# Performance work log

Hardware: AMD Instinct MI355X
Metric: run time of the kernel (lower is better)

Reference implementation:

```python
import jax, jax.numpy as jnp
import numpy as np

HEADS = 8
DEPTH = 2
LN_EPS = 1e-5


def _layernorm(x, g, b):
    m = jnp.mean(x, axis=-1, keepdims=True)
    v = jnp.var(x, axis=-1, keepdims=True)
    return (x - m) / jnp.sqrt(v + LN_EPS) * g + b


def setup_inputs() -> dict:
    key = jax.random.key(0)
    ks = jax.random.split(key, 16)
    b, c, n, t = 4, 64, 512, 12
    L, H = DEPTH, 256  # depth, mlp_dim
    s = 0.05
    return {
        'x': jax.random.normal(ks[0], (b, c, n, t), jnp.float32),
        'adj': jax.random.uniform(ks[1], (n, n), jnp.float32) / n,
        'pos': 0.02 * jax.random.normal(ks[2], (1, n, c), jnp.float32),
        'qkv_w': s * jax.random.normal(ks[3], (L, 3 * c, c), jnp.float32),
        'proj_w': s * jax.random.normal(ks[4], (L, c, c), jnp.float32),
        'proj_b': jnp.zeros((L, c), jnp.float32),
        'ln_g': jnp.ones((L, c), jnp.float32),
        'ln_b': jnp.zeros((L, c), jnp.float32),
        'ff_w1': s * jax.random.normal(ks[5], (L, H, c), jnp.float32),
        'ff_b1': jnp.zeros((L, H), jnp.float32),
        'ff_w2': s * jax.random.normal(ks[6], (L, c, H), jnp.float32),
        'ff_b2': jnp.zeros((L, c), jnp.float32),
        'gcn_w': s * jax.random.normal(ks[7], (L, c, 3 * c), jnp.float32),  # Conv2d 1x1: [c_out, 3*c_in]
        'gcn_b': jnp.zeros((L, c), jnp.float32),
    }


def reference(x, adj, pos, qkv_w, proj_w, proj_b, ln_g, ln_b,
              ff_w1, ff_b1, ff_w2, ff_b2, gcn_w, gcn_b):
    b, c, n, t = x.shape
    hd = c // HEADS
    scale = hd ** (-0.5)
    # [b, c, n, t] -> [b*t, n, c]
    h = jnp.transpose(x, (0, 3, 2, 1)).reshape(b * t, n, c) + pos
    for l in range(DEPTH):
        residual = h.reshape(b, t, n, c)
        # --- manual MHA (no pre-norm around attention, faithful to source) ---
        qkv = jnp.einsum('bnc,oc->bno', h, qkv_w[l])  # [bt, n, 3c]
        qkv = qkv.reshape(b * t, n, 3, HEADS, hd).transpose(2, 0, 3, 1, 4)
        q, k, v = qkv[0], qkv[1], qkv[2]  # [bt, heads, n, hd]
        attn = jax.nn.softmax(jnp.einsum('bhnd,bhmd->bhnm', q, k) * scale, axis=-1)
        o = jnp.einsum('bhnm,bhmd->bhnd', attn, v)
        o = o.transpose(0, 2, 1, 3).reshape(b * t, n, c)
        o = jnp.einsum('bnc,oc->bno', o, proj_w[l]) + proj_b[l]
        h = o + h
        # --- PreNorm FeedForward ---
        y = _layernorm(h, ln_g[l], ln_b[l])
        y = jax.nn.gelu(jnp.einsum('bnc,hc->bnh', y, ff_w1[l]) + ff_b1[l], approximate=False)
        y = jnp.einsum('bnh,ch->bnc', y, ff_w2[l]) + ff_b2[l]
        h = y + h
        # --- GCN on residual (order=2 diffusion) ---
        r = jnp.transpose(residual, (0, 3, 2, 1))  # [b, c, n, t]
        x1 = jnp.einsum('bcvt,vw->bcwt', r, adj)
        x2 = jnp.einsum('bcvt,vw->bcwt', x1, adj)
        cat = jnp.concatenate([r, x1, x2], axis=1)  # [b, 3c, n, t]
        g = jnp.einsum('bknt,ok->bont', cat, gcn_w[l]) + gcn_b[l][None, :, None, None]
        h = jnp.transpose(g, (0, 3, 2, 1)).reshape(b * t, n, c) + h
    return jnp.transpose(h.reshape(b, t, n, c), (0, 3, 2, 1))
```

## Files before the change

### kernel.cpp

```cpp
#include <hip/hip_runtime.h>
#include <math.h>


typedef __fp16 half_t;
typedef __attribute__((ext_vector_type(2))) __fp16 half2v;
typedef __attribute__((ext_vector_type(4))) __fp16 half4v;
typedef __attribute__((ext_vector_type(4))) float f32x4;

union PU  { half2v h2[2]; half4v h4; };
union F4H { float4 f; half4v h[2]; };
union F2H { float2 f2; half4v h4; };

#define ATS 72
#define BTS 68
#define KLS 20
#define QLS 20
#define VTS 516

__global__ __launch_bounds__(256) void k_pre(const float* __restrict__ x,
                                             const float* __restrict__ pos,
                                             const float* __restrict__ adj,
                                             const float* __restrict__ qkv_w,
                                             const float* __restrict__ proj_w,
                                             const float* __restrict__ ff_w1,
                                             const float* __restrict__ ff_w2,
                                             const float* __restrict__ gcn_w,
                                             float* __restrict__ h,
                                             half_t* __restrict__ hh,
                                             half_t* __restrict__ adjTh,
                                             half_t* __restrict__ wh,
                                             half_t* __restrict__ adjT2h) {
    __shared__ __align__(16) char smem[17920];
    float* t = (float*)smem;
    int tid = threadIdx.x;
    int bidx = blockIdx.x;
    if (bidx < 384) {
        int b = bidx / 96, vt0 = (bidx % 96) * 64;
#pragma unroll
        for (int i = 0; i < 4; ++i) {
            int g = tid + i * 256;
            int r = g >> 4, q = g & 15;
            *(float4*)&t[r * 65 + 4 * q] =
                *(const float4*)(x + ((size_t)(b * 64 + r)) * 6144 + vt0 + 4 * q);
        }
        __syncthreads();
#pragma unroll
        for (int i = 0; i < 4; ++i) {
            int g = tid + i * 256;
            int r = g >> 4, q = g & 15;
            int vt = vt0 + r;
            int v = vt / 12, tt = vt - v * 12;
            float4 pv = *(const float4*)(pos + v * 64 + 4 * q);
            float4 o;
            o.x = t[(4 * q + 0) * 65 + r] + pv.x;
            o.y = t[(4 * q + 1) * 65 + r] + pv.y;
            o.z = t[(4 * q + 2) * 65 + r] + pv.z;
            o.w = t[(4 * q + 3) * 65 + r] + pv.w;
            size_t idx = ((size_t)((b * 12 + tt) * 512 + v)) * 64 + 4 * q;
            *(float4*)(h + idx) = o;
            PU u;
            u.h2[0] = __builtin_amdgcn_cvt_pkrtz(o.x, o.y);
            u.h2[1] = __builtin_amdgcn_cvt_pkrtz(o.z, o.w);
            *(half4v*)(hh + idx) = u.h4;
        }
    } else if (bidx < 448) {
        int fb = bidx - 384;
        int v0 = (fb & 7) * 64, w0 = (fb >> 3) * 64;
#pragma unroll
        for (int i = 0; i < 4; ++i) {
            int g = tid + i * 256;
            int r = g >> 4, q = g & 15;
            float4 a = *(const float4*)(adj + (size_t)(v0 + r) * 512 + w0 + 4 * q);
            t[(4 * q + 0) * 65 + r] = a.x;
            t[(4 * q + 1) * 65 + r] = a.y;
            t[(4 * q + 2) * 65 + r] = a.z;
            t[(4 * q + 3) * 65 + r] = a.w;
        }
        __syncthreads();
#pragma unroll
        for (int i = 0; i < 4; ++i) {
            int g = tid + i * 256;
            int rw = g >> 4, q = g & 15;
            const float* src = &t[rw * 65 + 4 * q];
            PU u;
            u.h2[0] = __builtin_amdgcn_cvt_pkrtz(src[0], src[1]);
            u.h2[1] = __builtin_amdgcn_cvt_pkrtz(src[2], src[3]);
            *(half4v*)(adjTh + (size_t)(w0 + rw) * 512 + v0 + 4 * q) = u.h4;
        }
    } else if (bidx < 928) {
        int i = (bidx - 448) * 256 + tid;
        float v;
        if (i < 24576) v = qkv_w[i];
        else if (i < 32768) v = proj_w[i - 24576];
        else if (i < 65536) v = ff_w1[i - 32768];
        else if (i < 98304) v = ff_w2[i - 65536];
        else v = gcn_w[i - 98304];
        wh[i] = (half_t)v;
    } else {
        half_t* a_t = (half_t*)smem;
        half_t* b_t = (half_t*)smem + 64 * ATS;
        int fb = bidx - 928;
        int w0 = (fb & 7) * 64, v0 = (fb >> 3) * 64;
        int wave = tid >> 6, lane = tid & 63;
        int lm = lane & 15, lg = lane >> 4;
        const f32x4 zc = {0.f, 0.f, 0.f, 0.f};
        f32x4 acc[4] = {zc, zc, zc, zc};
        for (int kc = 0; kc < 8; ++kc) {
#pragma unroll
            for (int i = 0; i < 4; ++i) {
                int g = tid + i * 256;
                int uu = g >> 4, q = g & 15;
                float4 a = *(const float4*)(adj + (size_t)(kc * 64 + uu) * 512 + w0 + 4 * q);
                a_t[(4 * q + 0) * ATS + uu] = (half_t)a.x;
                a_t[(4 * q + 1) * ATS + uu] = (half_t)a.y;
                a_t[(4 * q + 2) * ATS + uu] = (half_t)a.z;
                a_t[(4 * q + 3) * ATS + uu] = (half_t)a.w;
            }
#pragma unroll
            for (int i = 0; i < 4; ++i) {
                int g = tid + i * 256;
                int c = g >> 4, q = g & 15;
                float4 a = *(const float4*)(adj + (size_t)(v0 + c) * 512 + kc * 64 + 4 * q);
                PU u;
                u.h2[0] = __builtin_amdgcn_cvt_pkrtz(a.x, a.y);
                u.h2[1] = __builtin_amdgcn_cvt_pkrtz(a.z, a.w);
                *(half4v*)&b_t[c * BTS + 4 * q] = u.h4;
            }
            __syncthreads();
#pragma unroll
            for (int k16 = 0; k16 < 4; ++k16) {
                half4v af = *(const half4v*)&a_t[(wave * 16 + lm) * ATS + k16 * 16 + lg * 4];
#pragma unroll
                for (int nt = 0; nt < 4; ++nt) {
                    half4v bf = *(const half4v*)&b_t[(nt * 16 + lm) * BTS + k16 * 16 + lg * 4];
                    acc[nt] = __builtin_amdgcn_mfma_f32_16x16x16f16(af, bf, acc[nt], 0, 0, 0);
                }
            }
            __syncthreads();
        }
#pragma unroll
        for (int nt = 0; nt < 4; ++nt)
#pragma unroll
            for (int r = 0; r < 4; ++r)
                adjT2h[(size_t)(w0 + wave * 16 + lg * 4 + r) * 512 + v0 + nt * 16 + lm] =
                    (half_t)acc[nt][r];
    }
}

__global__ __launch_bounds__(256) void k_qd(const half_t* __restrict__ hh,
                                            const half_t* __restrict__ Wh,
                                            half_t* __restrict__ qh,
                                            half_t* __restrict__ kh,
                                            half_t* __restrict__ vh,
                                            const half_t* __restrict__ adjTh,
                                            const half_t* __restrict__ adjT2h,
                                            half_t* __restrict__ x1h,
                                            half_t* __restrict__ x2h) {
    __shared__ __align__(16) half_t sbuf[2 * 64 * ATS + 64 * BTS];
    int tid = threadIdx.x;
    int bidx = blockIdx.x;
    int wave = tid >> 6, lane = tid & 63;
    int lm = lane & 15, lg = lane >> 4;
    const f32x4 zc = {0.f, 0.f, 0.f, 0.f};

    if (bidx < 384) {
        int wid = bidx * 4 + wave;
        int row = wid * 16 + lm;
        half4v xf[4];
#pragma unroll
        for (int kc = 0; kc < 4; ++kc) {
            F2H u;
            u.f2 = *(const float2*)(hh + (size_t)row * 64 + kc * 16 + lg * 4);
            xf[kc] = u.h4;
        }
        const float SC = 0.35355339059327373f * 1.4426950408889634f;
        int bt = row >> 9, v = row & 511;
        half4v wf[4];
#pragma unroll
        for (int kc = 0; kc < 4; ++kc)
            wf[kc] = *(const half4v*)(Wh + (size_t)lm * 64 + kc * 16 + lg * 4);
#pragma unroll
        for (int nt = 0; nt < 12; ++nt) {
            half4v cw[4];
#pragma unroll
            for (int kc = 0; kc < 4; ++kc) cw[kc] = wf[kc];
            if (nt < 11) {
#pragma unroll
                for (int kc = 0; kc < 4; ++kc)
                    wf[kc] = *(const half4v*)(Wh + (size_t)((nt + 1) * 16 + lm) * 64 + kc * 16 + lg * 4);
            }
            f32x4 acc = zc;
#pragma unroll
            for (int kc = 0; kc < 4; ++kc)
                acc = __builtin_amdgcn_mfma_f32_16x16x16f16(cw[kc], xf[kc], acc, 0, 0, 0);
            int s = nt >> 2;
            if (s == 0) { acc[0] *= SC; acc[1] *= SC; acc[2] *= SC; acc[3] *= SC; }
            int head = ((nt & 3) << 1) + (lg >> 1);
            int d0 = (lg & 1) * 4;
            PU o2;
            o2.h2[0] = __builtin_amdgcn_cvt_pkrtz(acc[0], acc[1]);
            o2.h2[1] = __builtin_amdgcn_cvt_pkrtz(acc[2], acc[3]);
            half_t* dst = (s == 0) ? qh : ((s == 1) ? kh : vh);
            *(half4v*)(dst + ((size_t)(bt * 8 + head) * 512 + v) * 8 + d0) = o2.h4;
        }
    } else {
        half_t* a_t  = sbuf;
        half_t* a2_t = sbuf + 64 * ATS;
        half_t* b_t  = sbuf + 2 * 64 * ATS;
        int fb = bidx - 384;
        int w0 = (fb & 7) * 64;
        int bt = fb >> 3;
        f32x4 acc0[4] = {zc, zc, zc, zc};
        f32x4 acc1[4] = {zc, zc, zc, zc};
        for (int kc = 0; kc < 8; ++kc) {
#pragma unroll
            for (int i = 0; i < 4; ++i) {
                int g = tid + i * 256;
                if (g < 512) {
                    int r = g >> 3, s = g & 7;
                    *(float4*)&a_t[r * ATS + s * 8] =
                        *(const float4*)(adjTh + (size_t)(w0 + r) * 512 + kc * 64 + s * 8);
                } else {
                    int g2 = g - 512;
                    int r = g2 >> 3, s = g2 & 7;
                    *(float4*)&a2_t[r * ATS + s * 8] =
                        *(const float4*)(adjT2h + (size_t)(w0 + r) * 512 + kc * 64 + s * 8);
                }
            }
#pragma unroll
            for (int i = 0; i < 2; ++i) {
                int g = tid + i * 256;
                int vr = g >> 3, s = g & 7;
                F4H u;
                u.f = *(const float4*)(hh + ((size_t)(bt * 512 + kc * 64 + vr)) * 64 + s * 8);
#pragma unroll
                for (int e = 0; e < 8; ++e)
                    b_t[(s * 8 + e) * BTS + vr] = u.h[e >> 2][e & 3];
            }
            __syncthreads();
#pragma unroll
            for (int k16 = 0; k16 < 4; ++k16) {
                half4v af0 = *(const half4v*)&a_t[(wave * 16 + lm) * ATS + k16 * 16 + lg * 4];
                half4v af1 = *(const half4v*)&a2_t[(wave * 16 + lm) * ATS + k16 * 16 + lg * 4];
#pragma unroll
                for (int nt = 0; nt < 4; ++nt) {
                    half4v bf = *(const half4v*)&b_t[(nt * 16 + lm) * BTS + k16 * 16 + lg * 4];
                    acc0[nt] = __builtin_amdgcn_mfma_f32_16x16x16f16(af0, bf, acc0[nt], 0, 0, 0);
                    acc1[nt] = __builtin_amdgcn_mfma_f32_16x16x16f16(af1, bf, acc1[nt], 0, 0, 0);
                }
            }
            __syncthreads();
        }
#pragma unroll
        for (int nt = 0; nt < 4; ++nt)
#pragma unroll
            for (int r = 0; r < 4; ++r) {
                size_t o = (size_t)(w0 + wave * 16 + lg * 4 + r) * 3072 + bt * 64 + nt * 16 + lm;
                x1h[o] = (half_t)acc0[nt][r];
                x2h[o] = (half_t)acc1[nt][r];
            }
    }
}

__global__ __launch_bounds__(512) void k_ag(const half_t* __restrict__ qh,
                                            const half_t* __restrict__ kh,
                                            const half_t* __restrict__ vh,
                                            half_t* __restrict__ obh,
                                            const half_t* __restrict__ hh,
                                            const half_t* __restrict__ x1h,
                                            const half_t* __restrict__ x2h,
                                            const half_t* __restrict__ Wh,
                                            const float* __restrict__ bias,
                                            float* __restrict__ gout) {
    __shared__ __align__(16) half_t sbuf[512 * KLS + 16 * VTS + 256 * QLS];
    int tid = threadIdx.x;
    int bidx = blockIdx.x;
    const half4v zero4 = {(__fp16)0.f, (__fp16)0.f, (__fp16)0.f, (__fp16)0.f};
    const f32x4 zc = {0.f, 0.f, 0.f, 0.f};

    if (bidx < 768) {
        half_t* kl = sbuf;
        half_t* vt = sbuf + 512 * KLS;
        half_t* ql = sbuf + 512 * KLS + 16 * VTS;
        int bh = bidx >> 1;
        int half_ = bidx & 1;
        const half_t* kbase = kh + (size_t)bh * 4096;
        const half_t* vbase = vh + (size_t)bh * 4096;
        const half_t* qbase = qh + (size_t)bh * 4096 + half_ * 2048;

        if (tid < 256) {
#pragma unroll
            for (int kk = 0; kk < 2; ++kk) {
                int key = tid * 2 + kk;
                F4H u;
                u.f = *(const float4*)(kbase + key * 8);
                half4v* rowp = (half4v*)&kl[key * KLS];
                rowp[0] = u.h[0];
                rowp[1] = u.h[1];
                rowp[2] = zero4;
                rowp[3] = zero4;
            }
            {
                F4H u;
                u.f = *(const float4*)(qbase + tid * 8);
                half4v* rowp = (half4v*)&ql[tid * QLS];
                rowp[0] = u.h[0];
                rowp[1] = u.h[1];
                rowp[2] = zero4;
                rowp[3] = zero4;
            }
            {
                int k0 = tid * 2;
                F4H a, b;
                a.f = *(const float4*)(vbase + k0 * 8);
                b.f = *(const float4*)(vbase + k0 * 8 + 8);
#pragma unroll
                for (int d = 0; d < 8; ++d) {
                    half2v p = {a.h[d >> 2][d & 3], b.h[d >> 2][d & 3]};
                    *(half2v*)&vt[d * VTS + k0] = p;
                }
            }
        }
        for (int i = tid; i < 1032; i += 512)
            ((half4v*)(vt + 8 * VTS))[i] = zero4;
        __syncthreads();

        int wave = tid >> 6, lane = tid & 63;
        int lm = lane & 15, lg = lane >> 4;
        int bt = bh >> 3, head = bh & 7;

#pragma unroll 1
        for (int st = 0; st < 2; ++st) {
            int qrow0 = wave * 32 + st * 16;
            half4v qf = *(const half4v*)&ql[(qrow0 + lm) * QLS + lg * 4];
            f32x4 acc = zc;
            float l0 = 0.f, l1 = 0.f, l2 = 0.f, l3 = 0.f;
#pragma unroll 4
            for (int kt = 0; kt < 32; ++kt) {
                int key0 = kt * 16;
                half4v ka = *(const half4v*)&kl[(key0 + lm) * KLS + lg * 4];
                f32x4 c1 = __builtin_amdgcn_mfma_f32_16x16x16f16(ka, qf, zc, 0, 0, 0);
                float p0 = exp2f(fminf(c1[0], 12.f));
                float p1 = exp2f(fminf(c1[1], 12.f));
                float p2 = exp2f(fminf(c1[2], 12.f));
                float p3 = exp2f(fminf(c1[3], 12.f));
                l0 += p0; l1 += p1; l2 += p2; l3 += p3;
                PU pu;
                pu.h2[0] = __builtin_amdgcn_cvt_pkrtz(p0, p1);
                pu.h2[1] = __builtin_amdgcn_cvt_pkrtz(p2, p3);
                half4v va = *(const half4v*)&vt[lm * VTS + key0 + lg * 4];
                acc = __builtin_amdgcn_mfma_f32_16x16x16f16(va, pu.h4, acc, 0, 0, 0);
            }
            float lsum = (l0 + l1) + (l2 + l3);
            lsum += __shfl_xor(lsum, 16);
            lsum += __shfl_xor(lsum, 32);
            if (lg < 2) {
                float inv = 1.f / lsum;
                int rowg = half_ * 256 + qrow0 + lm;
                PU o2;
                o2.h2[0] = __builtin_amdgcn_cvt_pkrtz(acc[0] * inv, acc[1] * inv);
                o2.h2[1] = __builtin_amdgcn_cvt_pkrtz(acc[2] * inv, acc[3] * inv);
                *(half4v*)(obh + ((size_t)(bt * 512 + rowg)) * 64 + head * 8 + lg * 4) = o2.h4;
            }
        }
    } else {
        half_t* a_t = sbuf;
        half_t* b_t = sbuf + 64 * ATS;
        int row0 = (bidx - 768) * 64;
        int wave = tid >> 6, lane = tid & 63;
        int lm = lane & 15, lg = lane >> 4;
        f32x4 acc[4] = {zc, zc, zc, zc};

        for (int ch = 0; ch < 3; ++ch) {
            if (tid < 256) {
                if (ch == 0) {
#pragma unroll
                    for (int i = 0; i < 2; ++i) {
                        int g = tid + i * 256;
                        int r = g >> 3, s = g & 7;
                        int rowg = row0 + r;
                        int v = rowg / 48, bt = rowg - v * 48;
                        *(float4*)&a_t[r * ATS + s * 8] =
                            *(const float4*)(hh + ((size_t)(bt * 512 + v)) * 64 + s * 8);
                    }
                } else {
                    const half_t* X = (ch == 1) ? x1h : x2h;
#pragma unroll
                    for (int i = 0; i < 2; ++i) {
                        int g = tid + i * 256;
                        int r = g >> 3, s = g & 7;
                        *(float4*)&a_t[r * ATS + s * 8] =
                            *(const float4*)(X + (size_t)(row0 + r) * 64 + s * 8);
                    }
                }
#pragma unroll
                for (int i = 0; i < 4; ++i) {
                    int g = tid + i * 256;
                    int r = g >> 4, q = g & 15;
                    *(half4v*)&b_t[r * BTS + 4 * q] =
                        *(const half4v*)(Wh + (size_t)r * 192 + ch * 64 + 4 * q);
                }
            }
            __syncthreads();
            if (tid < 256) {
#pragma unroll
                for (int k16 = 0; k16 < 4; ++k16) {
                    half4v af = *(const half4v*)&a_t[(wave * 16 + lm) * ATS + k16 * 16 + lg * 4];
#pragma unroll
                    for (int nt = 0; nt < 4; ++nt) {
                        half4v bf = *(const half4v*)&b_t[(nt * 16 + lm) * BTS + k16 * 16 + lg * 4];
                        acc[nt] = __builtin_amdgcn_mfma_f32_16x16x16f16(bf, af, acc[nt], 0, 0, 0);
                    }
                }
            }
            __syncthreads();
        }
        if (tid < 256) {
            int row = row0 + wave * 16 + lm;
            int v = row / 48, bt = row - v * 48;
            float* gp = gout + ((size_t)(bt * 512 + v)) * 64;
#pragma unroll
            for (int nt = 0; nt < 4; ++nt) {
                float4 bb = *(const float4*)(bias + nt * 16 + lg * 4);
                *(float4*)(gp + nt * 16 + lg * 4) =
                    make_float4(acc[nt][0] + bb.x, acc[nt][1] + bb.y,
                                acc[nt][2] + bb.z, acc[nt][3] + bb.w);
            }
        }
    }
}

__global__ __launch_bounds__(128) void k_plf(const half_t* __restrict__ obh,
                                             const half_t* __restrict__ pwh,
                                             const float* __restrict__ pb,
                                             const float* __restrict__ g,
                                             const float* __restrict__ bln,
                                             const half_t* __restrict__ w1h,
                                             const float* __restrict__ b1,
                                             const half_t* __restrict__ w2h,
                                             const float* __restrict__ b2,
                                             const float* __restrict__ gout,
                                             float* __restrict__ h,
                                             half_t* __restrict__ hh,
                                             float* __restrict__ out,
                                             int last) {
    int wid = blockIdx.x * 2 + (threadIdx.x >> 6);
    int lane = threadIdx.x & 63;
    int lm = lane & 15, lg = lane >> 4;
    int row = wid * 16 + lm;
    const f32x4 zc = {0.f, 0.f, 0.f, 0.f};

    half4v pf[4];
#pragma unroll
    for (int kc = 0; kc < 4; ++kc)
        pf[kc] = *(const half4v*)(pwh + (size_t)lm * 64 + kc * 16 + lg * 4);

    half4v of[4];
#pragma unroll
    for (int kc = 0; kc < 4; ++kc) {
        F2H u;
        u.f2 = *(const float2*)(obh + (size_t)row * 64 + kc * 16 + lg * 4);
        of[kc] = u.h4;
    }

    f32x4 hp[4];
#pragma unroll
    for (int nt = 0; nt < 4; ++nt) {
        half4v cw[4];
#pragma unroll
        for (int kc = 0; kc < 4; ++kc) cw[kc] = pf[kc];
        if (nt < 3) {
#pragma unroll
            for (int kc = 0; kc < 4; ++kc)
                pf[kc] = *(const half4v*)(pwh + (size_t)((nt + 1) * 16 + lm) * 64 + kc * 16 + lg * 4);
        }
        f32x4 c = zc;
#pragma unroll
        for (int kc = 0; kc < 4; ++kc)
            c = __builtin_amdgcn_mfma_f32_16x16x16f16(cw[kc], of[kc], c, 0, 0, 0);
        float4 ho = *(const float4*)(h + (size_t)row * 64 + nt * 16 + lg * 4);
        float4 bb = *(const float4*)(pb + nt * 16 + lg * 4);
        hp[nt][0] = c[0] + ho.x + bb.x;
        hp[nt][1] = c[1] + ho.y + bb.y;
        hp[nt][2] = c[2] + ho.z + bb.z;
        hp[nt][3] = c[3] + ho.w + bb.w;
    }

    float s = 0.f, s2 = 0.f;
#pragma unroll
    for (int nt = 0; nt < 4; ++nt)
#pragma unroll
        for (int r = 0; r < 4; ++r) {
            s += hp[nt][r];
            s2 += hp[nt][r] * hp[nt][r];
        }
    s += __shfl_xor(s, 16);  s2 += __shfl_xor(s2, 16);
    s += __shfl_xor(s, 32);  s2 += __shfl_xor(s2, 32);
    float mean = s * (1.f / 64.f);
    float var = s2 * (1.f / 64.f) - mean * mean;
    float rstd = rsqrtf(var + 1e-5f);

    half4v xf[4];
#pragma unroll
    for (int nt = 0; nt < 4; ++nt) {
        float4 gg = *(const float4*)(g + nt * 16 + lg * 4);
        float4 bb = *(const float4*)(bln + nt * 16 + lg * 4);
        float y0 = (hp[nt][0] - mean) * rstd * gg.x + bb.x;
        float y1 = (hp[nt][1] - mean) * rstd * gg.y + bb.y;
        float y2 = (hp[nt][2] - mean) * rstd * gg.z + bb.z;
        float y3 = (hp[nt][3] - mean) * rstd * gg.w + bb.w;
        PU u;
        u.h2[0] = __builtin_amdgcn_cvt_pkrtz(y0, y1);
        u.h2[1] = __builtin_amdgcn_cvt_pkrtz(y2, y3);
        xf[nt] = u.h4;
    }

    half4v w1f[4];
#pragma unroll
    for (int kc = 0; kc < 4; ++kc)
        w1f[kc] = *(const half4v*)(w1h + (size_t)lm * 64 + kc * 16 + lg * 4);

    f32x4 acc[4] = {zc, zc, zc, zc};
#pragma unroll 4
    for (int ht = 0; ht < 16; ++ht) {
        half4v cw[4];
#pragma unroll
        for (int kc = 0; kc < 4; ++kc) cw[kc] = w1f[kc];
        half4v w2f[4];
#pragma unroll
        for (int ot = 0; ot < 4; ++ot)
            w2f[ot] = *(const half4v*)(w2h + (size_t)(ot * 16 + lm) * 256 + ht * 16 + lg * 4);
        if (ht < 15) {
#pragma unroll
            for (int kc = 0; kc < 4; ++kc)
                w1f[kc] = *(const half4v*)(w1h + (size_t)((ht + 1) * 16 + lm) * 64 + kc * 16 + lg * 4);
        }
        f32x4 c1 = zc;
#pragma unroll
        for (int kc = 0; kc < 4; ++kc)
            c1 = __builtin_amdgcn_mfma_f32_16x16x16f16(cw[kc], xf[kc], c1, 0, 0, 0);
        float4 bb = *(const float4*)(b1 + ht * 16 + lg * 4);
        float y0 = c1[0] + bb.x;
        float y1 = c1[1] + bb.y;
        float y2 = c1[2] + bb.z;
        float y3 = c1[3] + bb.w;
        y0 = 0.5f * y0 * (1.0f + erff(y0 * 0.70710678118654752f));
        y1 = 0.5f * y1 * (1.0f + erff(y1 * 0.70710678118654752f));
        y2 = 0.5f * y2 * (1.0f + erff(y2 * 0.70710678118654752f));
        y3 = 0.5f * y3 * (1.0f + erff(y3 * 0.70710678118654752f));
        PU p;
        p.h2[0] = __builtin_amdgcn_cvt_pkrtz(y0, y1);
        p.h2[1] = __builtin_amdgcn_cvt_pkrtz(y2, y3);
#pragma unroll
        for (int ot = 0; ot < 4; ++ot)
            acc[ot] = __builtin_amdgcn_mfma_f32_16x16x16f16(w2f[ot], p.h4, acc[ot], 0, 0, 0);
    }

    if (!last) {
#pragma unroll
        for (int ot = 0; ot < 4; ++ot) {
            float4 bb = *(const float4*)(b2 + ot * 16 + lg * 4);
            float4 gv = *(const float4*)(gout + (size_t)row * 64 + ot * 16 + lg * 4);
            float4 fv = make_float4(hp[ot][0] + acc[ot][0] + bb.x + gv.x,
                                    hp[ot][1] + acc[ot][1] + bb.y + gv.y,
                                    hp[ot][2] + acc[ot][2] + bb.z + gv.z,
                                    hp[ot][3] + acc[ot][3] + bb.w + gv.w);
            size_t idx = (size_t)row * 64 + ot * 16 + lg * 4;
            *(float4*)(h + idx) = fv;
            PU u;
            u.h2[0] = __builtin_amdgcn_cvt_pkrtz(fv.x, fv.y);
            u.h2[1] = __builtin_amdgcn_cvt_pkrtz(fv.z, fv.w);
            *(half4v*)(hh + idx) = u.h4;
        }
    } else {
        int bt = row >> 9, v = row & 511;
        int b = bt / 12, t = bt - b * 12;
        float* op = out + (size_t)b * 393216 + v * 12 + t;
#pragma unroll
        for (int ot = 0; ot < 4; ++ot) {
            float4 bb = *(const float4*)(b2 + ot * 16 + lg * 4);
            float4 gv = *(const float4*)(gout + (size_t)row * 64 + ot * 16 + lg * 4);
            int c0 = ot * 16 + lg * 4;
            op[(size_t)(c0 + 0) * 6144] = hp[ot][0] + acc[ot][0] + bb.x + gv.x;
            op[(size_t)(c0 + 1) * 6144] = hp[ot][1] + acc[ot][1] + bb.y + gv.y;
            op[(size_t)(c0 + 2) * 6144] = hp[ot][2] + acc[ot][2] + bb.z + gv.z;
            op[(size_t)(c0 + 3) * 6144] = hp[ot][3] + acc[ot][3] + bb.w + gv.w;
        }
    }
}

extern "C" void kernel_launch(void* const* d_in, const int* in_sizes, int n_in,
                              void* d_out, int out_size, void* d_ws, size_t ws_size,
                              hipStream_t stream) {
    const float* x      = (const float*)d_in[0];
    const float* adj    = (const float*)d_in[1];
    const float* pos    = (const float*)d_in[2];
    const float* qkv_w  = (const float*)d_in[3];
    const float* proj_w = (const float*)d_in[4];
    const float* proj_b = (const float*)d_in[5];
    const float* ln_g   = (const float*)d_in[6];
    const float* ln_b   = (const float*)d_in[7];
    const float* ff_w1  = (const float*)d_in[8];
    const float* ff_b1  = (const float*)d_in[9];
    const float* ff_w2  = (const float*)d_in[10];
    const float* ff_b2  = (const float*)d_in[11];
    const float* gcn_w  = (const float*)d_in[12];
    const float* gcn_b  = (const float*)d_in[13];
    float* out = (float*)d_out;

    const size_t SZ = 1572864;
    float* h    = (float*)d_ws;
    float* gout = h + SZ;
    half_t* hh  = (half_t*)(gout + SZ);
    half_t* x1h = hh + SZ;
    half_t* x2h = x1h + SZ;
    half_t* qh  = x2h + SZ;
    half_t* kh  = qh + SZ;
    half_t* vh  = kh + SZ;
    half_t* obh = vh + SZ;
    half_t* adjTh  = obh + SZ;
    half_t* adjT2h = adjTh + 262144;
    half_t* wh     = adjT2h + 262144;
    half_t* qkv_wh  = wh;
    half_t* proj_wh = wh + 24576;
    half_t* ff_w1h  = wh + 32768;
    half_t* ff_w2h  = wh + 65536;
    half_t* gcn_wh  = wh + 98304;

    k_pre<<<992, 256, 0, stream>>>(x, pos, adj, qkv_w, proj_w, ff_w1, ff_w2, gcn_w,
                                   h, hh, adjTh, wh, adjT2h);
    for (int l = 0; l < 2; ++l) {
        k_qd<<<768, 256, 0, stream>>>(hh, qkv_wh + l * 12288, qh, kh, vh,
                                      adjTh, adjT2h, x1h, x2h);
        k_ag<<<1152, 512, 0, stream>>>(qh, kh, vh, obh, hh, x1h, x2h,
                                       gcn_wh + l * 12288, gcn_b + l * 64, gout);
        k_plf<<<768, 128, 0, stream>>>(obh, proj_wh + l * 4096, proj_b + l * 64,
                                       ln_g + l * 64, ln_b + l * 64,
                                       ff_w1h + l * 16384, ff_b1 + l * 256,
                                       ff_w2h + l * 16384, ff_b2 + l * 64, gout, h, hh,
                                       out, l);
    }
}
```

Baseline: 275.3 us.

## Fuse GCN 1x1 conv into diffusion kernel and vectorize weight conversion

Fuses the GCN channel-mixing matmul into the adjacency diffusion blocks of k_qd. The x1/x2 tiles stay in shared memory next to the residual tile and are multiplied by the GCN weights directly, removing the x1h/x2h global round-trip and the separate GEMM blocks in k_ag. k_ag now only does attention with 768 blocks. The weight-to-fp16 conversion in k_pre is vectorized to float4, which cuts its block count. The trade-off is more shared memory and register pressure in k_qd, plus GCN weights read straight from global memory per block.

```diff
diff --git a/kernel.cpp b/kernel.cpp
--- a/kernel.cpp
+++ b/kernel.cpp
@@ -16,6 +16,7 @@
 #define KLS 20
 #define QLS 20
 #define VTS 516
+#define CTS 200
 
 __global__ __launch_bounds__(256) void k_pre(const float* __restrict__ x,
                                              const float* __restrict__ pos,
@@ -87,19 +88,22 @@
             u.h2[1] = __builtin_amdgcn_cvt_pkrtz(src[2], src[3]);
             *(half4v*)(adjTh + (size_t)(w0 + rw) * 512 + v0 + 4 * q) = u.h4;
         }
-    } else if (bidx < 928) {
-        int i = (bidx - 448) * 256 + tid;
-        float v;
-        if (i < 24576) v = qkv_w[i];
-        else if (i < 32768) v = proj_w[i - 24576];
-        else if (i < 65536) v = ff_w1[i - 32768];
-        else if (i < 98304) v = ff_w2[i - 65536];
-        else v = gcn_w[i - 98304];
-        wh[i] = (half_t)v;
+    } else if (bidx < 568) {
+        int i = ((bidx - 448) * 256 + tid) * 4;
+        float4 v;
+        if (i < 24576) v = *(const float4*)(qkv_w + i);
+        else if (i < 32768) v = *(const float4*)(proj_w + (i - 24576));
+        else if (i < 65536) v = *(const float4*)(ff_w1 + (i - 32768));
+        else if (i < 98304) v = *(const float4*)(ff_w2 + (i - 65536));
+        else v = *(const float4*)(gcn_w + (i - 98304));
+        PU u;
+        u.h2[0] = __builtin_amdgcn_cvt_pkrtz(v.x, v.y);
+        u.h2[1] = __builtin_amdgcn_cvt_pkrtz(v.z, v.w);
+        *(half4v*)(wh + i) = u.h4;
     } else {
         half_t* a_t = (half_t*)smem;
         half_t* b_t = (half_t*)smem + 64 * ATS;
-        int fb = bidx - 928;
+        int fb = bidx - 568;
         int w0 = (fb & 7) * 64, v0 = (fb >> 3) * 64;
         int wave = tid >> 6, lane = tid & 63;
         int lm = lane & 15, lg = lane >> 4;
@@ -154,8 +158,9 @@
                                             half_t* __restrict__ vh,
                                             const half_t* __restrict__ adjTh,
                                             const half_t* __restrict__ adjT2h,
-                                            half_t* __restrict__ x1h,
-                                            half_t* __restrict__ x2h) {
+                                            const half_t* __restrict__ Wg,
+                                            const float* __restrict__ gb,
+                                            float* __restrict__ gout) {
     __shared__ __align__(16) half_t sbuf[2 * 64 * ATS + 64 * BTS];
     int tid = threadIdx.x;
     int bidx = blockIdx.x;
@@ -251,181 +256,137 @@
             }
             __syncthreads();
         }
+        half_t* cat_t = sbuf;
 #pragma unroll
         for (int nt = 0; nt < 4; ++nt)
 #pragma unroll
             for (int r = 0; r < 4; ++r) {
-                size_t o = (size_t)(w0 + wave * 16 + lg * 4 + r) * 3072 + bt * 64 + nt * 16 + lm;
-                x1h[o] = (half_t)acc0[nt][r];
-                x2h[o] = (half_t)acc1[nt][r];
-            }
+                int vrow = wave * 16 + lg * 4 + r;
+                cat_t[vrow * CTS + 64  + nt * 16 + lm] = (half_t)acc0[nt][r];
+                cat_t[vrow * CTS + 128 + nt * 16 + lm] = (half_t)acc1[nt][r];
+            }
+#pragma unroll
+        for (int i = 0; i < 2; ++i) {
+            int g = tid + i * 256;
+            int r = g >> 3, s = g & 7;
+            *(float4*)&cat_t[r * CTS + s * 8] =
+                *(const float4*)(hh + ((size_t)(bt * 512 + w0 + r)) * 64 + s * 8);
+        }
+        __syncthreads();
+        f32x4 gacc[4] = {zc, zc, zc, zc};
+#pragma unroll
+        for (int k16 = 0; k16 < 12; ++k16) {
+            half4v cf = *(const half4v*)&cat_t[(wave * 16 + lm) * CTS + k16 * 16 + lg * 4];
+#pragma unroll
+            for (int nt = 0; nt < 4; ++nt) {
+                half4v wf = *(const half4v*)(Wg + (size_t)(nt * 16 + lm) * 192 + k16 * 16 + lg * 4);
+                gacc[nt] = __builtin_amdgcn_mfma_f32_16x16x16f16(wf, cf, gacc[nt], 0, 0, 0);
+            }
+        }
+        int grow = bt * 512 + w0 + wave * 16 + lm;
+        float* gp = gout + (size_t)grow * 64;
+#pragma unroll
+        for (int nt = 0; nt < 4; ++nt) {
+            float4 bb = *(const float4*)(gb + nt * 16 + lg * 4);
+            *(float4*)(gp + nt * 16 + lg * 4) =
+                make_float4(gacc[nt][0] + bb.x, gacc[nt][1] + bb.y,
+                            gacc[nt][2] + bb.z, gacc[nt][3] + bb.w);
+        }
     }
 }
 
 __global__ __launch_bounds__(512) void k_ag(const half_t* __restrict__ qh,
                                             const half_t* __restrict__ kh,
                                             const half_t* __restrict__ vh,
-                                            half_t* __restrict__ obh,
-                                            const half_t* __restrict__ hh,
-                                            const half_t* __restrict__ x1h,
-                                            const half_t* __restrict__ x2h,
-                                            const half_t* __restrict__ Wh,
-                                            const float* __restrict__ bias,
-                                            float* __restrict__ gout) {
+                                            half_t* __restrict__ obh) {
     __shared__ __align__(16) half_t sbuf[512 * KLS + 16 * VTS + 256 * QLS];
     int tid = threadIdx.x;
     int bidx = blockIdx.x;
     const half4v zero4 = {(__fp16)0.f, (__fp16)0.f, (__fp16)0.f, (__fp16)0.f};
     const f32x4 zc = {0.f, 0.f, 0.f, 0.f};
 
-    if (bidx < 768) {
-        half_t* kl = sbuf;
-        half_t* vt = sbuf + 512 * KLS;
-        half_t* ql = sbuf + 512 * KLS + 16 * VTS;
-        int bh = bidx >> 1;
-        int half_ = bidx & 1;
-        const half_t* kbase = kh + (size_t)bh * 4096;
-        const half_t* vbase = vh + (size_t)bh * 4096;
-        const half_t* qbase = qh + (size_t)bh * 4096 + half_ * 2048;
-
-        if (tid < 256) {
-#pragma unroll
-            for (int kk = 0; kk < 2; ++kk) {
-                int key = tid * 2 + kk;
-                F4H u;
-                u.f = *(const float4*)(kbase + key * 8);
-                half4v* rowp = (half4v*)&kl[key * KLS];
-                rowp[0] = u.h[0];
-                rowp[1] = u.h[1];
-                rowp[2] = zero4;
-                rowp[3] = zero4;
-            }
-            {
-                F4H u;
-                u.f = *(const float4*)(qbase + tid * 8);
-                half4v* rowp = (half4v*)&ql[tid * QLS];
-                rowp[0] = u.h[0];
-                rowp[1] = u.h[1];
-                rowp[2] = zero4;
-                rowp[3] = zero4;
-            }
-            {
-                int k0 = tid * 2;
-                F4H a, b;
-                a.f = *(const float4*)(vbase + k0 * 8);
-                b.f = *(const float4*)(vbase + k0 * 8 + 8);
-#pragma unroll
-                for (int d = 0; d < 8; ++d) {
-                    half2v p = {a.h[d >> 2][d & 3], b.h[d >> 2][d & 3]};
-                    *(half2v*)&vt[d * VTS + k0] = p;
-                }
-            }
-        }
-        for (int i = tid; i < 1032; i += 512)
-            ((half4v*)(vt + 8 * VTS))[i] = zero4;
-        __syncthreads();
-
-        int wave = tid >> 6, lane = tid & 63;
-        int lm = lane & 15, lg = lane >> 4;
-        int bt = bh >> 3, head = bh & 7;
+    half_t* kl = sbuf;
+    half_t* vt = sbuf + 512 * KLS;
+    half_t* ql = sbuf + 512 * KLS + 16 * VTS;
+    int bh = bidx >> 1;
+    int half_ = bidx & 1;
+    const half_t* kbase = kh + (size_t)bh * 4096;
+    const half_t* vbase = vh + (size_t)bh * 4096;
+    const half_t* qbase = qh + (size_t)bh * 4096 + half_ * 2048;
+
+    if (tid < 256) {
+#pragma unroll
+        for (int kk = 0; kk < 2; ++kk) {
+            int key = tid * 2 + kk;
+            F4H u;
+            u.f = *(const float4*)(kbase + key * 8);
+            half4v* rowp = (half4v*)&kl[key * KLS];
+            rowp[0] = u.h[0];
+            rowp[1] = u.h[1];
+            rowp[2] = zero4;
+            rowp[3] = zero4;
+        }
+        {
+            F4H u;
+            u.f = *(const float4*)(qbase + tid * 8);
+            half4v* rowp = (half4v*)&ql[tid * QLS];
+            rowp[0] = u.h[0];
+            rowp[1] = u.h[1];
+            rowp[2] = zero4;
+            rowp[3] = zero4;
+        }
+        {
+            int k0 = tid * 2;
+            F4H a, b;
+            a.f = *(const float4*)(vbase + k0 * 8);
+            b.f = *(const float4*)(vbase + k0 * 8 + 8);
+#pragma unroll
+            for (int d = 0; d < 8; ++d) {
+                half2v p = {a.h[d >> 2][d & 3], b.h[d >> 2][d & 3]};
+                *(half2v*)&vt[d * VTS + k0] = p;
+            }
+        }
+    }
+    for (int i = tid; i < 1032; i += 512)
+        ((half4v*)(vt + 8 * VTS))[i] = zero4;
+    __syncthreads();
+
+    int wave = tid >> 6, lane = tid & 63;
+    int lm = lane & 15, lg = lane >> 4;
+    int bt = bh >> 3, head = bh & 7;
 
 #pragma unroll 1
-        for (int st = 0; st < 2; ++st) {
-            int qrow0 = wave * 32 + st * 16;
-            half4v qf = *(const half4v*)&ql[(qrow0 + lm) * QLS + lg * 4];
-            f32x4 acc = zc;
-            float l0 = 0.f, l1 = 0.f, l2 = 0.f, l3 = 0.f;
+    for (int st = 0; st < 2; ++st) {
+        int qrow0 = wave * 32 + st * 16;
+        half4v qf = *(const half4v*)&ql[(qrow0 + lm) * QLS + lg * 4];
+        f32x4 acc = zc;
+        float l0 = 0.f, l1 = 0.f, l2 = 0.f, l3 = 0.f;
 #pragma unroll 4
-            for (int kt = 0; kt < 32; ++kt) {
-                int key0 = kt * 16;
-                half4v ka = *(const half4v*)&kl[(key0 + lm) * KLS + lg * 4];
-                f32x4 c1 = __builtin_amdgcn_mfma_f32_16x16x16f16(ka, qf, zc, 0, 0, 0);
-                float p0 = exp2f(fminf(c1[0], 12.f));
-                float p1 = exp2f(fminf(c1[1], 12.f));
-                float p2 = exp2f(fminf(c1[2], 12.f));
-                float p3 = exp2f(fminf(c1[3], 12.f));
-                l0 += p0; l1 += p1; l2 += p2; l3 += p3;
-                PU pu;
-                pu.h2[0] = __builtin_amdgcn_cvt_pkrtz(p0, p1);
-                pu.h2[1] = __builtin_amdgcn_cvt_pkrtz(p2, p3);
-                half4v va = *(const half4v*)&vt[lm * VTS + key0 + lg * 4];
-                acc = __builtin_amdgcn_mfma_f32_16x16x16f16(va, pu.h4, acc, 0, 0, 0);
-            }
-            float lsum = (l0 + l1) + (l2 + l3);
-            lsum += __shfl_xor(lsum, 16);
-            lsum += __shfl_xor(lsum, 32);
-            if (lg < 2) {
-                float inv = 1.f / lsum;
-                int rowg = half_ * 256 + qrow0 + lm;
-                PU o2;
-                o2.h2[0] = __builtin_amdgcn_cvt_pkrtz(acc[0] * inv, acc[1] * inv);
-                o2.h2[1] = __builtin_amdgcn_cvt_pkrtz(acc[2] * inv, acc[3] * inv);
-                *(half4v*)(obh + ((size_t)(bt * 512 + rowg)) * 64 + head * 8 + lg * 4) = o2.h4;
-            }
-        }
-    } else {
-        half_t* a_t = sbuf;
-        half_t* b_t = sbuf + 64 * ATS;
-        int row0 = (bidx - 768) * 64;
-        int wave = tid >> 6, lane = tid & 63;
-        int lm = lane & 15, lg = lane >> 4;
-        f32x4 acc[4] = {zc, zc, zc, zc};
-
-        for (int ch = 0; ch < 3; ++ch) {
-            if (tid < 256) {
-                if (ch == 0) {
-#pragma unroll
-                    for (int i = 0; i < 2; ++i) {
-                        int g = tid + i * 256;
-                        int r = g >> 3, s = g & 7;
-                        int rowg = row0 + r;
-                        int v = rowg / 48, bt = rowg - v * 48;
-                        *(float4*)&a_t[r * ATS + s * 8] =
-                            *(const float4*)(hh + ((size_t)(bt * 512 + v)) * 64 + s * 8);
-                    }
-                } else {
-                    const half_t* X = (ch == 1) ? x1h : x2h;
-#pragma unroll
-                    for (int i = 0; i < 2; ++i) {
-                        int g = tid + i * 256;
-                        int r = g >> 3, s = g & 7;
-                        *(float4*)&a_t[r * ATS + s * 8] =
-                            *(const float4*)(X + (size_t)(row0 + r) * 64 + s * 8);
-                    }
-                }
-#pragma unroll
-                for (int i = 0; i < 4; ++i) {
-                    int g = tid + i * 256;
-                    int r = g >> 4, q = g & 15;
-                    *(half4v*)&b_t[r * BTS + 4 * q] =
-                        *(const half4v*)(Wh + (size_t)r * 192 + ch * 64 + 4 * q);
-                }
-            }
-            __syncthreads();
-            if (tid < 256) {
-#pragma unroll
-                for (int k16 = 0; k16 < 4; ++k16) {
-                    half4v af = *(const half4v*)&a_t[(wave * 16 + lm) * ATS + k16 * 16 + lg * 4];
-#pragma unroll
-                    for (int nt = 0; nt < 4; ++nt) {
-                        half4v bf = *(const half4v*)&b_t[(nt * 16 + lm) * BTS + k16 * 16 + lg * 4];
-                        acc[nt] = __builtin_amdgcn_mfma_f32_16x16x16f16(bf, af, acc[nt], 0, 0, 0);
-                    }
-                }
-            }
-            __syncthreads();
-        }
-        if (tid < 256) {
-            int row = row0 + wave * 16 + lm;
-            int v = row / 48, bt = row - v * 48;
-            float* gp = gout + ((size_t)(bt * 512 + v)) * 64;
-#pragma unroll
-            for (int nt = 0; nt < 4; ++nt) {
-                float4 bb = *(const float4*)(bias + nt * 16 + lg * 4);
-                *(float4*)(gp + nt * 16 + lg * 4) =
-                    make_float4(acc[nt][0] + bb.x, acc[nt][1] + bb.y,
-                                acc[nt][2] + bb.z, acc[nt][3] + bb.w);
-            }
+        for (int kt = 0; kt < 32; ++kt) {
+            int key0 = kt * 16;
+            half4v ka = *(const half4v*)&kl[(key0 + lm) * KLS + lg * 4];
+            f32x4 c1 = __builtin_amdgcn_mfma_f32_16x16x16f16(ka, qf, zc, 0, 0, 0);
+            float p0 = exp2f(fminf(c1[0], 12.f));
+            float p1 = exp2f(fminf(c1[1], 12.f));
+            float p2 = exp2f(fminf(c1[2], 12.f));
+            float p3 = exp2f(fminf(c1[3], 12.f));
+            l0 += p0; l1 += p1; l2 += p2; l3 += p3;
+            PU pu;
+            pu.h2[0] = __builtin_amdgcn_cvt_pkrtz(p0, p1);
+            pu.h2[1] = __builtin_amdgcn_cvt_pkrtz(p2, p3);
+            half4v va = *(const half4v*)&vt[lm * VTS + key0 + lg * 4];
+            acc = __builtin_amdgcn_mfma_f32_16x16x16f16(va, pu.h4, acc, 0, 0, 0);
+        }
+        float lsum = (l0 + l1) + (l2 + l3);
+        lsum += __shfl_xor(lsum, 16);
+        lsum += __shfl_xor(lsum, 32);
+        if (lg < 2) {
+            float inv = 1.f / lsum;
+            int rowg = half_ * 256 + qrow0 + lm;
+            PU o2;
+            o2.h2[0] = __builtin_amdgcn_cvt_pkrtz(acc[0] * inv, acc[1] * inv);
+            o2.h2[1] = __builtin_amdgcn_cvt_pkrtz(acc[2] * inv, acc[3] * inv);
+            *(half4v*)(obh + ((size_t)(bt * 512 + rowg)) * 64 + head * 8 + lg * 4) = o2.h4;
         }
     }
 }
@@ -626,14 +587,15 @@
     half_t* ff_w1h  = wh + 32768;
     half_t* ff_w2h  = wh + 65536;
     half_t* gcn_wh  = wh + 98304;
-
-    k_pre<<<992, 256, 0, stream>>>(x, pos, adj, qkv_w, proj_w, ff_w1, ff_w2, gcn_w,
+    (void)x1h; (void)x2h;
+
+    k_pre<<<632, 256, 0, stream>>>(x, pos, adj, qkv_w, proj_w, ff_w1, ff_w2, gcn_w,
                                    h, hh, adjTh, wh, adjT2h);
     for (int l = 0; l < 2; ++l) {
         k_qd<<<768, 256, 0, stream>>>(hh, qkv_wh + l * 12288, qh, kh, vh,
-                                      adjTh, adjT2h, x1h, x2h);
-        k_ag<<<1152, 512, 0, stream>>>(qh, kh, vh, obh, hh, x1h, x2h,
-                                       gcn_wh + l * 12288, gcn_b + l * 64, gout);
+                                      adjTh, adjT2h,
+                                      gcn_wh + l * 12288, gcn_b + l * 64, gout);
+        k_ag<<<768, 512, 0, stream>>>(qh, kh, vh, obh);
         k_plf<<<768, 128, 0, stream>>>(obh, proj_wh + l * 4096, proj_b + l * 64,
                                        ln_g + l * 64, ln_b + l * 64,
                                        ff_w1h + l * 16384, ff_b1 + l * 256,
```

Result: slower. 292.7 us (+6.3%).

## Split FFN hidden dim across wave pairs, use all waves in GCN GEMM, vectorize weight cast

Applied to the files above, without the earlier changes.

The FFN kernel now runs two waves per 16-row tile, each taking half of the 256 hidden units, and combines their partial second-GEMM outputs through shared memory with one barrier. The GCN output GEMM branch of the attention kernel now uses all eight waves of its 512-thread block, each computing two of the four 16-column output tiles, where before half the block sat idle. The weight fp16 conversion uses float4 loads and packed conversion, which cuts its block count from 480 to 120. The costs are an extra LDS exchange and barrier in the FFN kernel, and each wave reloading the same shared-memory A fragments.

```diff
diff --git a/kernel.cpp b/kernel.cpp
--- a/kernel.cpp
+++ b/kernel.cpp
@@ -87,19 +87,22 @@
             u.h2[1] = __builtin_amdgcn_cvt_pkrtz(src[2], src[3]);
             *(half4v*)(adjTh + (size_t)(w0 + rw) * 512 + v0 + 4 * q) = u.h4;
         }
-    } else if (bidx < 928) {
-        int i = (bidx - 448) * 256 + tid;
-        float v;
-        if (i < 24576) v = qkv_w[i];
-        else if (i < 32768) v = proj_w[i - 24576];
-        else if (i < 65536) v = ff_w1[i - 32768];
-        else if (i < 98304) v = ff_w2[i - 65536];
-        else v = gcn_w[i - 98304];
-        wh[i] = (half_t)v;
+    } else if (bidx < 568) {
+        int i = ((bidx - 448) * 256 + tid) * 4;
+        float4 v;
+        if (i < 24576) v = *(const float4*)(qkv_w + i);
+        else if (i < 32768) v = *(const float4*)(proj_w + (i - 24576));
+        else if (i < 65536) v = *(const float4*)(ff_w1 + (i - 32768));
+        else if (i < 98304) v = *(const float4*)(ff_w2 + (i - 65536));
+        else v = *(const float4*)(gcn_w + (i - 98304));
+        PU u;
+        u.h2[0] = __builtin_amdgcn_cvt_pkrtz(v.x, v.y);
+        u.h2[1] = __builtin_amdgcn_cvt_pkrtz(v.z, v.w);
+        *(half4v*)(wh + i) = u.h4;
     } else {
         half_t* a_t = (half_t*)smem;
         half_t* b_t = (half_t*)smem + 64 * ATS;
-        int fb = bidx - 928;
+        int fb = bidx - 568;
         int w0 = (fb & 7) * 64, v0 = (fb >> 3) * 64;
         int wave = tid >> 6, lane = tid & 63;
         int lm = lane & 15, lg = lane >> 4;
@@ -369,68 +372,62 @@
         int row0 = (bidx - 768) * 64;
         int wave = tid >> 6, lane = tid & 63;
         int lm = lane & 15, lg = lane >> 4;
-        f32x4 acc[4] = {zc, zc, zc, zc};
+        int wr = wave & 3;
+        int wn = wave >> 2;
+        f32x4 acc[2] = {zc, zc};
 
         for (int ch = 0; ch < 3; ++ch) {
-            if (tid < 256) {
+            {
+                int g = tid;
+                int r = g >> 3, s = g & 7;
                 if (ch == 0) {
-#pragma unroll
-                    for (int i = 0; i < 2; ++i) {
-                        int g = tid + i * 256;
-                        int r = g >> 3, s = g & 7;
-                        int rowg = row0 + r;
-                        int v = rowg / 48, bt = rowg - v * 48;
-                        *(float4*)&a_t[r * ATS + s * 8] =
-                            *(const float4*)(hh + ((size_t)(bt * 512 + v)) * 64 + s * 8);
-                    }
+                    int rowg = row0 + r;
+                    int v = rowg / 48, bt = rowg - v * 48;
+                    *(float4*)&a_t[r * ATS + s * 8] =
+                        *(const float4*)(hh + ((size_t)(bt * 512 + v)) * 64 + s * 8);
                 } else {
                     const half_t* X = (ch == 1) ? x1h : x2h;
-#pragma unroll
-                    for (int i = 0; i < 2; ++i) {
-                        int g = tid + i * 256;
-                        int r = g >> 3, s = g & 7;
-                        *(float4*)&a_t[r * ATS + s * 8] =
-                            *(const float4*)(X + (size_t)(row0 + r) * 64 + s * 8);
-                    }
+                    *(float4*)&a_t[r * ATS + s * 8] =
+                        *(const float4*)(X + (size_t)(row0 + r) * 64 + s * 8);
                 }
-#pragma unroll
-                for (int i = 0; i < 4; ++i) {
-                    int g = tid + i * 256;
-                    int r = g >> 4, q = g & 15;
-                    *(half4v*)&b_t[r * BTS + 4 * q] =
-                        *(const half4v*)(Wh + (size_t)r * 192 + ch * 64 + 4 * q);
+            }
+#pragma unroll
+            for (int i = 0; i < 2; ++i) {
+                int g = tid + i * 512;
+                int r = g >> 4, q = g & 15;
+                *(half4v*)&b_t[r * BTS + 4 * q] =
+                    *(const half4v*)(Wh + (size_t)r * 192 + ch * 64 + 4 * q);
+            }
+            __syncthreads();
+#pragma unroll
+            for (int k16 = 0; k16 < 4; ++k16) {
+                half4v af = *(const half4v*)&a_t[(wr * 16 + lm) * ATS + k16 * 16 + lg * 4];
+#pragma unroll
+                for (int j = 0; j < 2; ++j) {
+                    int nt = wn * 2 + j;
+                    half4v bf = *(const half4v*)&b_t[(nt * 16 + lm) * BTS + k16 * 16 + lg * 4];
+                    acc[j] = __builtin_amdgcn_mfma_f32_16x16x16f16(bf, af, acc[j], 0, 0, 0);
                 }
             }
             __syncthreads();
-            if (tid < 256) {
-#pragma unroll
-                for (int k16 = 0; k16 < 4; ++k16) {
-                    half4v af = *(const half4v*)&a_t[(wave * 16 + lm) * ATS + k16 * 16 + lg * 4];
-#pragma unroll
-                    for (int nt = 0; nt < 4; ++nt) {
-                        half4v bf = *(const half4v*)&b_t[(nt * 16 + lm) * BTS + k16 * 16 + lg * 4];
-                        acc[nt] = __builtin_amdgcn_mfma_f32_16x16x16f16(bf, af, acc[nt], 0, 0, 0);
-                    }
-                }
-            }
-            __syncthreads();
-        }
-        if (tid < 256) {
-            int row = row0 + wave * 16 + lm;
+        }
+        {
+            int row = row0 + wr * 16 + lm;
             int v = row / 48, bt = row - v * 48;
             float* gp = gout + ((size_t)(bt * 512 + v)) * 64;
 #pragma unroll
-            for (int nt = 0; nt < 4; ++nt) {
+            for (int j = 0; j < 2; ++j) {
+                int nt = wn * 2 + j;
                 float4 bb = *(const float4*)(bias + nt * 16 + lg * 4);
                 *(float4*)(gp + nt * 16 + lg * 4) =
-                    make_float4(acc[nt][0] + bb.x, acc[nt][1] + bb.y,
-                                acc[nt][2] + bb.z, acc[nt][3] + bb.w);
+                    make_float4(acc[j][0] + bb.x, acc[j][1] + bb.y,
+                                acc[j][2] + bb.z, acc[j][3] + bb.w);
             }
         }
     }
 }
 
-__global__ __launch_bounds__(128) void k_plf(const half_t* __restrict__ obh,
+__global__ __launch_bounds__(256) void k_plf(const half_t* __restrict__ obh,
                                              const half_t* __restrict__ pwh,
                                              const float* __restrict__ pb,
                                              const float* __restrict__ g,
@@ -444,7 +441,11 @@
                                              half_t* __restrict__ hh,
                                              float* __restrict__ out,
                                              int last) {
-    int wid = blockIdx.x * 2 + (threadIdx.x >> 6);
+    __shared__ __align__(16) float sredf[2][2][64][8];
+    int wave = threadIdx.x >> 6;
+    int pairIdx = wave >> 1;
+    int sub = wave & 1;
+    int wid = blockIdx.x * 2 + pairIdx;
     int lane = threadIdx.x & 63;
     int lm = lane & 15, lg = lane >> 4;
     int row = wid * 16 + lm;
@@ -515,14 +516,16 @@
         xf[nt] = u.h4;
     }
 
+    int htBase = sub * 8;
     half4v w1f[4];
 #pragma unroll
     for (int kc = 0; kc < 4; ++kc)
-        w1f[kc] = *(const half4v*)(w1h + (size_t)lm * 64 + kc * 16 + lg * 4);
+        w1f[kc] = *(const half4v*)(w1h + (size_t)(htBase * 16 + lm) * 64 + kc * 16 + lg * 4);
 
     f32x4 acc[4] = {zc, zc, zc, zc};
 #pragma unroll 4
-    for (int ht = 0; ht < 16; ++ht) {
+    for (int t8 = 0; t8 < 8; ++t8) {
+        int ht = htBase + t8;
         half4v cw[4];
 #pragma unroll
         for (int kc = 0; kc < 4; ++kc) cw[kc] = w1f[kc];
@@ -530,7 +533,7 @@
 #pragma unroll
         for (int ot = 0; ot < 4; ++ot)
             w2f[ot] = *(const half4v*)(w2h + (size_t)(ot * 16 + lm) * 256 + ht * 16 + lg * 4);
-        if (ht < 15) {
+        if (t8 < 7) {
 #pragma unroll
             for (int kc = 0; kc < 4; ++kc)
                 w1f[kc] = *(const half4v*)(w1h + (size_t)((ht + 1) * 16 + lm) * 64 + kc * 16 + lg * 4);
@@ -556,15 +559,24 @@
             acc[ot] = __builtin_amdgcn_mfma_f32_16x16x16f16(w2f[ot], p.h4, acc[ot], 0, 0, 0);
     }
 
+    int po = 2 * (1 - sub);
+    *(f32x4*)&sredf[pairIdx][sub][lane][0] = acc[po];
+    *(f32x4*)&sredf[pairIdx][sub][lane][4] = acc[po + 1];
+    __syncthreads();
+    f32x4 tot[2];
+    tot[0] = acc[2 * sub]     + *(const f32x4*)&sredf[pairIdx][1 - sub][lane][0];
+    tot[1] = acc[2 * sub + 1] + *(const f32x4*)&sredf[pairIdx][1 - sub][lane][4];
+
     if (!last) {
 #pragma unroll
-        for (int ot = 0; ot < 4; ++ot) {
+        for (int j = 0; j < 2; ++j) {
+            int ot = 2 * sub + j;
             float4 bb = *(const float4*)(b2 + ot * 16 + lg * 4);
             float4 gv = *(const float4*)(gout + (size_t)row * 64 + ot * 16 + lg * 4);
-            float4 fv = make_float4(hp[ot][0] + acc[ot][0] + bb.x + gv.x,
-                                    hp[ot][1] + acc[ot][1] + bb.y + gv.y,
-                                    hp[ot][2] + acc[ot][2] + bb.z + gv.z,
-                                    hp[ot][3] + acc[ot][3] + bb.w + gv.w);
+            float4 fv = make_float4(hp[ot][0] + tot[j][0] + bb.x + gv.x,
+                                    hp[ot][1] + tot[j][1] + bb.y + gv.y,
+                                    hp[ot][2] + tot[j][2] + bb.z + gv.z,
+                                    hp[ot][3] + tot[j][3] + bb.w + gv.w);
             size_t idx = (size_t)row * 64 + ot * 16 + lg * 4;
             *(float4*)(h + idx) = fv;
             PU u;
@@ -577,14 +589,15 @@
         int b = bt / 12, t = bt - b * 12;
         float* op = out + (size_t)b * 393216 + v * 12 + t;
 #pragma unroll
-        for (int ot = 0; ot < 4; ++ot) {
+        for (int j = 0; j < 2; ++j) {
+            int ot = 2 * sub + j;
             float4 bb = *(const float4*)(b2 + ot * 16 + lg * 4);
             float4 gv = *(const float4*)(gout + (size_t)row * 64 + ot * 16 + lg * 4);
             int c0 = ot * 16 + lg * 4;
-            op[(size_t)(c0 + 0) * 6144] = hp[ot][0] + acc[ot][0] + bb.x + gv.x;
-            op[(size_t)(c0 + 1) * 6144] = hp[ot][1] + acc[ot][1] + bb.y + gv.y;
-            op[(size_t)(c0 + 2) * 6144] = hp[ot][2] + acc[ot][2] + bb.z + gv.z;
-            op[(size_t)(c0 + 3) * 6144] = hp[ot][3] + acc[ot][3] + bb.w + gv.w;
+            op[(size_t)(c0 + 0) * 6144] = hp[ot][0] + tot[j][0] + bb.x + gv.x;
+            op[(size_t)(c0 + 1) * 6144] = hp[ot][1] + tot[j][1] + bb.y + gv.y;
+            op[(size_t)(c0 + 2) * 6144] = hp[ot][2] + tot[j][2] + bb.z + gv.z;
+            op[(size_t)(c0 + 3) * 6144] = hp[ot][3] + tot[j][3] + bb.w + gv.w;
         }
     }
 }
@@ -627,14 +640,14 @@
     half_t* ff_w2h  = wh + 65536;
     half_t* gcn_wh  = wh + 98304;
 
-    k_pre<<<992, 256, 0, stream>>>(x, pos, adj, qkv_w, proj_w, ff_w1, ff_w2, gcn_w,
+    k_pre<<<632, 256, 0, stream>>>(x, pos, adj, qkv_w, proj_w, ff_w1, ff_w2, gcn_w,
                                    h, hh, adjTh, wh, adjT2h);
     for (int l = 0; l < 2; ++l) {
         k_qd<<<768, 256, 0, stream>>>(hh, qkv_wh + l * 12288, qh, kh, vh,
                                       adjTh, adjT2h, x1h, x2h);
         k_ag<<<1152, 512, 0, stream>>>(qh, kh, vh, obh, hh, x1h, x2h,
                                        gcn_wh + l * 12288, gcn_b + l * 64, gout);
-        k_plf<<<768, 128, 0, stream>>>(obh, proj_wh + l * 4096, proj_b + l * 64,
+        k_plf<<<768, 256, 0, stream>>>(obh, proj_wh + l * 4096, proj_b + l * 64,
                                        ln_g + l * 64, ln_b + l * 64,
                                        ff_w1h + l * 16384, ff_b1 + l * 256,
                                        ff_w2h + l * 16384, ff_b2 + l * 64, gout, h, hh,
```

Result: slower. 287.1 us (+4.3%).
